# Kernel tuning notes

Hardware: AMD Instinct MI355X
Metric: run time of the kernel (lower is better)

The kernel has to match this reference:

```python
import jax, jax.numpy as jnp
import numpy as np

B, N, NC, T, C, H = 8, 16, 16, 64, 512, 8


def setup_inputs() -> dict:
    key = jax.random.key(0)
    ks = jax.random.split(key, 7)
    s = 1.0 / np.sqrt(C)  # ~kaiming-uniform scale for Linear weights
    x = jax.random.normal(ks[0], (B, N, T, C), dtype=jnp.float32)
    c = jax.random.normal(ks[1], (B, NC, T, C), dtype=jnp.float32)
    mask = jax.random.randint(ks[2], (B, N * T, (N + NC) * T), 0, 2).astype(bool)
    Wq = jax.random.normal(ks[3], (C, C), dtype=jnp.float32) * s  # [out, in], torch Linear layout
    Wk = jax.random.normal(ks[4], (C, C), dtype=jnp.float32) * s
    Wv = jax.random.normal(ks[5], (C, C), dtype=jnp.float32) * s
    Wp = jax.random.normal(ks[6], (C, C), dtype=jnp.float32) * s
    return {"x": x, "c": c, "mask": mask, "Wq": Wq, "Wk": Wk, "Wv": Wv, "Wp": Wp}


def reference(x, c, mask, Wq, Wk, Wv, Wp):
    Bx, Nx, Tx, Cx = x.shape
    Dh = Cx // H
    kv_in = jnp.concatenate([x, c], axis=1)           # hybrid: [B, N+NC, T, C]
    Nk = kv_in.shape[1]
    # torch Linear: y = x @ W.T  -> einsum '...c,dc->...d'
    q = jnp.einsum('bntc,dc->bntd', x, Wq).reshape(Bx, Nx * Tx, H, Dh).transpose(0, 2, 1, 3)
    k = jnp.einsum('bntc,dc->bntd', kv_in, Wk).reshape(Bx, Nk * Tx, H, Dh).transpose(0, 2, 1, 3)
    v = jnp.einsum('bntc,dc->bntd', kv_in, Wv).reshape(Bx, Nk * Tx, H, Dh).transpose(0, 2, 1, 3)
    att = jnp.einsum('bhqd,bhkd->bhqk', q, k) * (1.0 / np.sqrt(Dh))  # [B,H,NT,NkT]
    att = jnp.where(mask[:, None, :, :], -jnp.inf, att)
    att = jax.nn.softmax(att, axis=-1)
    y = jnp.einsum('bhqk,bhkd->bhqd', att, v)          # [B,H,NT,Dh]
    y = y.transpose(0, 2, 1, 3).reshape(Bx, Nx * Tx, Cx)
    y = jnp.einsum('btc,dc->btd', y, Wp)
    return y.reshape(Bx, Nx, Tx, Cx)
```

## Files before the change

### kernel.cpp

```cpp
#include <hip/hip_runtime.h>
#include <hip/hip_bf16.h>
#include <stdint.h>

typedef __bf16 v8bf __attribute__((ext_vector_type(8)));
typedef short v4s __attribute__((ext_vector_type(4)));
typedef float f32x4 __attribute__((ext_vector_type(4)));
typedef float f32x2 __attribute__((ext_vector_type(2)));

__device__ __forceinline__ void gload_lds16(const void* g, void* l) {
    __builtin_amdgcn_global_load_lds(
        (const __attribute__((address_space(1))) void*)g,
        (__attribute__((address_space(3))) void*)l, 16, 0, 0);
}

__device__ __forceinline__ unsigned short f2bf(float f) {
    __hip_bfloat16 h = __float2bfloat16(f);
    return __builtin_bit_cast(unsigned short, h);
}

__device__ __forceinline__ float andf(float e, int m) {
    return __builtin_bit_cast(float, __builtin_bit_cast(unsigned int, e) & (unsigned int)m);
}

__device__ __forceinline__ int sbit(unsigned int w, int off) {
    int m;
    asm("v_bfe_i32 %0, %1, %2, 1" : "=v"(m) : "v"(w), "v"(off));
    return m;
}

#define WAITV4_BAR() asm volatile("s_waitcnt vmcnt(4)\n\ts_barrier" ::: "memory")
#define WAITV0_BAR() asm volatile("s_waitcnt vmcnt(0)\n\ts_barrier" ::: "memory")
#define RAW_BAR() asm volatile("s_barrier" ::: "memory")

__device__ __forceinline__ f32x4 mfma16x16x16bf(v4s a, v4s b, f32x4 c) {
#if __has_builtin(__builtin_amdgcn_mfma_f32_16x16x16bf16_1k)
    return __builtin_amdgcn_mfma_f32_16x16x16bf16_1k(a, b, c, 0, 0, 0);
#elif __has_builtin(__builtin_amdgcn_mfma_f32_16x16x16_bf16)
    return __builtin_amdgcn_mfma_f32_16x16x16_bf16(a, b, c, 0, 0, 0);
#else
    asm("s_nop 1\n\t"
        "v_mfma_f32_16x16x16_bf16 %0, %1, %2, %0\n\t"
        "s_nop 7\n\ts_nop 3"
        : "+v"(c) : "v"(a), "v"(b));
    return c;
#endif
}

__global__ __launch_bounds__(256) void cvt_xcw(const float* __restrict__ x,
                                               const float* __restrict__ c,
                                               const float* __restrict__ wq,
                                               const float* __restrict__ wk,
                                               const float* __restrict__ wv,
                                               const float* __restrict__ wp,
                                               __hip_bfloat16* __restrict__ xc,
                                               __hip_bfloat16* __restrict__ wout) {
    int bid = blockIdx.x;
    if (bid < 8192) {
        int i = bid * 256 + threadIdx.x;
        long e = (long)i * 4;
        int b = (int)(e >> 20);
        int rem = (int)(e & ((1 << 20) - 1));
        int r = rem >> 9;
        int col = rem & 511;
        const float* src = (r < 1024) ? (x + ((long)b << 19) + (long)r * 512 + col)
                                      : (c + ((long)b << 19) + (long)(r - 1024) * 512 + col);
        float4 v = *(const float4*)src;
        ushort4 o;
        o.x = f2bf(v.x); o.y = f2bf(v.y); o.z = f2bf(v.z); o.w = f2bf(v.w);
        ((ushort4*)xc)[i] = o;
    } else {
        int i = (bid - 8192) * 256 + threadIdx.x;
        int e = i * 4;
        int w = e >> 18;
        int off = e & ((1 << 18) - 1);
        const float* src = (w == 0 ? wq : w == 1 ? wk : w == 2 ? wv : wp) + off;
        float4 val = *(const float4*)src;
        ushort4 o;
        o.x = f2bf(val.x); o.y = f2bf(val.y); o.z = f2bf(val.z); o.w = f2bf(val.w);
        ((ushort4*)wout)[i] = o;
    }
}

__global__ __launch_bounds__(256) void cvt_mask(const int* __restrict__ mask,
                                                unsigned long long* __restrict__ mbt) {
    int t = threadIdx.x;
    long base = (long)blockIdx.x * 1024;
#pragma unroll
    for (int j = 0; j < 4; j++) {
        long i = base + j * 256 + t;
        int v = mask[i] == 0;
        unsigned long long bits = __ballot(v);
        if ((t & 63) == 0) {
            int b = (int)(i >> 21);
            int q = (int)((i >> 11) & 1023);
            int word = (int)((i >> 6) & 31);
            mbt[((long)b * 32 + word) * 1024 + q] = bits;
        }
    }
}

__global__ __launch_bounds__(256) void gemm_qkv(const __hip_bfloat16* __restrict__ A,
                                                const __hip_bfloat16* __restrict__ Bw,
                                                __hip_bfloat16* __restrict__ Qw,
                                                __hip_bfloat16* __restrict__ Kw,
                                                __hip_bfloat16* __restrict__ Vtw) {
    __shared__ union {
        struct { __hip_bfloat16 As[2][128 * 32]; __hip_bfloat16 Bs[2][128 * 32]; } s;
        __hip_bfloat16 T[64 * 138];
    } u;
    const int tid = threadIdx.x;
    const int wave = tid >> 6, lane = tid & 63;
    const int m0 = blockIdx.x * 128, n0 = blockIdx.y * 128;

    const bool isQ = (blockIdx.y < 4);
    const int rr_base = m0 & 2047;
    if (isQ && rr_base >= 1024) return;

    const int la = lane >> 2;
    const int kc = (lane & 3) * 8;
    const long ga0 = (long)(m0 + wave * 16 + la) * 512 + kc;
    const long ga1 = (long)(m0 + (wave + 4) * 16 + la) * 512 + kc;
    const long gb0 = (long)(n0 + wave * 16 + la) * 512 + kc;
    const long gb1 = (long)(n0 + (wave + 4) * 16 + la) * 512 + kc;

    f32x4 acc[4][4] = {};
    const int mw = (wave & 1) * 64, nw = (wave >> 1) * 64;
    const int lrow = lane & 15, lk = (lane >> 4) * 8;

    gload_lds16(A + ga0, &u.s.As[0][wave * 512]);
    gload_lds16(A + ga1, &u.s.As[0][(wave + 4) * 512]);
    gload_lds16(Bw + gb0, &u.s.Bs[0][wave * 512]);
    gload_lds16(Bw + gb1, &u.s.Bs[0][(wave + 4) * 512]);

    for (int it = 0; it < 16; ++it) {
        const int cur = it & 1;
        if (it < 15) {
            const int k0 = (it + 1) * 32;
            gload_lds16(A + ga0 + k0, &u.s.As[cur ^ 1][wave * 512]);
            gload_lds16(A + ga1 + k0, &u.s.As[cur ^ 1][(wave + 4) * 512]);
            gload_lds16(Bw + gb0 + k0, &u.s.Bs[cur ^ 1][wave * 512]);
            gload_lds16(Bw + gb1 + k0, &u.s.Bs[cur ^ 1][(wave + 4) * 512]);
            WAITV4_BAR();
        } else {
            WAITV0_BAR();
        }
        v8bf a[4], b[4];
#pragma unroll
        for (int i = 0; i < 4; i++) {
            a[i] = *(const v8bf*)&u.s.As[cur][(mw + i * 16 + lrow) * 32 + lk];
            b[i] = *(const v8bf*)&u.s.Bs[cur][(nw + i * 16 + lrow) * 32 + lk];
        }
        __builtin_amdgcn_s_setprio(1);
#pragma unroll
        for (int mi = 0; mi < 4; mi++)
#pragma unroll
            for (int ni = 0; ni < 4; ni++)
                acc[mi][ni] = __builtin_amdgcn_mfma_f32_16x16x32_bf16(a[mi], b[ni], acc[mi][ni], 0, 0, 0);
        __builtin_amdgcn_s_setprio(0);
        RAW_BAR();
    }

    const int lq = lane >> 4;
    const int b_ = m0 >> 11;
    if (blockIdx.y < 8) {
        const float qs = isQ ? 0.1803368801f : 1.f;
#pragma unroll
        for (int pass = 0; pass < 2; ++pass) {
            if (pass) __syncthreads();
            if ((wave & 1) == pass) {
#pragma unroll
                for (int mi = 0; mi < 4; mi++)
#pragma unroll
                    for (int ni = 0; ni < 4; ni++) {
                        const int nl = nw + ni * 16 + lrow;
#pragma unroll
                        for (int r = 0; r < 4; r++)
                            u.T[(mi * 16 + lq * 4 + r) * 138 + nl] =
                                __float2bfloat16(acc[mi][ni][r] * qs);
                    }
            }
            __syncthreads();
#pragma unroll
            for (int i = 0; i < 4; i++) {
                int sI = tid + i * 256;
                int row = sI >> 4, ch = sI & 15;
                int grow = m0 + pass * 64 + row;
                int rr = grow & 2047;
                int gcol = n0 + ch * 8;
                int h = (gcol & 511) >> 6, dh = gcol & 63;
                uint4 v = *(const uint4*)&u.T[row * 138 + ch * 8];
                if (isQ)
                    *(uint4*)&Qw[((long)(b_ * 8 + h) * 1024 + rr) * 64 + dh] = v;
                else
                    *(uint4*)&Kw[((long)(b_ * 8 + h) * 2048 + rr) * 64 + dh] = v;
            }
        }
    } else {
        const int no = (blockIdx.y - 8) * 128;
        const int rrb = m0 & 2047;
#pragma unroll
        for (int pass = 0; pass < 2; ++pass) {
            __syncthreads();
            if ((wave >> 1) == pass) {
#pragma unroll
                for (int mi = 0; mi < 4; mi++)
#pragma unroll
                    for (int ni = 0; ni < 4; ni++) {
                        int n_l = ni * 16 + lrow;
                        int m_l = mw + mi * 16 + lq * 4;
                        ushort4 pk;
                        pk.x = f2bf(acc[mi][ni][0]); pk.y = f2bf(acc[mi][ni][1]);
                        pk.z = f2bf(acc[mi][ni][2]); pk.w = f2bf(acc[mi][ni][3]);
                        *(ushort4*)&u.T[n_l * 136 + m_l] = pk;
                    }
            }
            __syncthreads();
#pragma unroll
            for (int i = 0; i < 4; i++) {
                int sI = tid + i * 256;
                int n_l = sI >> 4, ch = sI & 15;
                int ng = no + pass * 64 + n_l;
                int h = ng >> 6, dh = ng & 63;
                uint4 v = *(const uint4*)&u.T[n_l * 136 + ch * 8];
                *(uint4*)&Vtw[((long)(b_ * 8 + h) * 64 + dh) * 2048 + rrb + ch * 8] = v;
            }
        }
    }
}

__global__ __launch_bounds__(256) void gemm_out(const __hip_bfloat16* __restrict__ A,
                                                const __hip_bfloat16* __restrict__ Bw,
                                                float* __restrict__ outp) {
    __shared__ __hip_bfloat16 As[2][128 * 32];
    __shared__ __hip_bfloat16 Bs[2][128 * 32];
    const int tid = threadIdx.x;
    const int wave = tid >> 6, lane = tid & 63;
    const int m0 = blockIdx.x * 128, n0 = blockIdx.y * 128;

    const int la = lane >> 2;
    const int kc = (lane & 3) * 8;
    const long ga0 = (long)(m0 + wave * 16 + la) * 512 + kc;
    const long ga1 = (long)(m0 + (wave + 4) * 16 + la) * 512 + kc;
    const long gb0 = (long)(n0 + wave * 16 + la) * 512 + kc;
    const long gb1 = (long)(n0 + (wave + 4) * 16 + la) * 512 + kc;

    f32x4 acc[4][4] = {};
    const int mw = (wave & 1) * 64, nw = (wave >> 1) * 64;
    const int lrow = lane & 15, lk = (lane >> 4) * 8;

    gload_lds16(A + ga0, &As[0][wave * 512]);
    gload_lds16(A + ga1, &As[0][(wave + 4) * 512]);
    gload_lds16(Bw + gb0, &Bs[0][wave * 512]);
    gload_lds16(Bw + gb1, &Bs[0][(wave + 4) * 512]);

    for (int it = 0; it < 16; ++it) {
        const int cur = it & 1;
        if (it < 15) {
            const int k0 = (it + 1) * 32;
            gload_lds16(A + ga0 + k0, &As[cur ^ 1][wave * 512]);
            gload_lds16(A + ga1 + k0, &As[cur ^ 1][(wave + 4) * 512]);
            gload_lds16(Bw + gb0 + k0, &Bs[cur ^ 1][wave * 512]);
            gload_lds16(Bw + gb1 + k0, &Bs[cur ^ 1][(wave + 4) * 512]);
            WAITV4_BAR();
        } else {
            WAITV0_BAR();
        }
        v8bf a[4], b[4];
#pragma unroll
        for (int i = 0; i < 4; i++) {
            a[i] = *(const v8bf*)&As[cur][(mw + i * 16 + lrow) * 32 + lk];
            b[i] = *(const v8bf*)&Bs[cur][(nw + i * 16 + lrow) * 32 + lk];
        }
        __builtin_amdgcn_s_setprio(1);
#pragma unroll
        for (int mi = 0; mi < 4; mi++)
#pragma unroll
            for (int ni = 0; ni < 4; ni++)
                acc[mi][ni] = __builtin_amdgcn_mfma_f32_16x16x32_bf16(a[mi], b[ni], acc[mi][ni], 0, 0, 0);
        __builtin_amdgcn_s_setprio(0);
        RAW_BAR();
    }

    const int lq = lane >> 4;
#pragma unroll
    for (int mi = 0; mi < 4; mi++)
#pragma unroll
        for (int ni = 0; ni < 4; ni++)
#pragma unroll
            for (int r = 0; r < 4; r++) {
                int grow = m0 + mw + mi * 16 + lq * 4 + r;
                int gcol = n0 + nw + ni * 16 + lrow;
                outp[(long)grow * 512 + gcol] = acc[mi][ni][r];
            }
}

__global__ __launch_bounds__(256) void flash(const __hip_bfloat16* __restrict__ Q,
                                             const __hip_bfloat16* __restrict__ K,
                                             const __hip_bfloat16* __restrict__ Vt,
                                             const unsigned long long* __restrict__ Mbt,
                                             __hip_bfloat16* __restrict__ Y) {
    constexpr int LDT = 72;
    __shared__ __hip_bfloat16 Ks[2][64 * LDT];
    __shared__ __hip_bfloat16 Vts[2][64 * LDT];

    const int L = blockIdx.x;
    const int b = L & 7, qt = (L >> 3) & 15, h = L >> 7;
    const int bh = b * 8 + h;
    const int tid = threadIdx.x, w = tid >> 6, lane = tid & 63;
    const int lcol = lane & 15, lq = lane >> 4;

    const __hip_bfloat16* Qp = Q + ((long)bh * 1024 + qt * 64 + w * 16 + lcol) * 64 + lq * 8;
    const __hip_bfloat16* Kg = K + (long)bh * 2048 * 64;
    const __hip_bfloat16* Vg = Vt + (long)bh * 64 * 2048;
    const unsigned long long* Mp = Mbt + (long)b * 32 * 1024 + qt * 64 + w * 16 + lcol;

    const int u0 = tid, u1 = tid + 256;
    const int r0 = u0 >> 3, p0 = u0 & 7;
    const int r1 = u1 >> 3, p1 = u1 & 7;

    int boff[8];
#pragma unroll
    for (int jj = 0; jj < 8; jj++)
        boff[jj] = (jj >> 2) * 16 + lq * 4 + (jj & 3);

    v8bf bq0 = *(const v8bf*)(Qp);
    v8bf bq1 = *(const v8bf*)(Qp + 32);

    f32x4 O[4] = {};
    f32x2 ls = {0.f, 0.f};

    unsigned long long mword = Mp[0];
    {
        const uint4* ksrc = (const uint4*)Kg;
        uint4 k0 = ksrc[u0], k1 = ksrc[u1];
        uint4 v0 = *(const uint4*)(Vg + (long)r0 * 2048 + p0 * 8);
        uint4 v1 = *(const uint4*)(Vg + (long)r1 * 2048 + p1 * 8);
        *(uint4*)&Ks[0][r0 * LDT + p0 * 8] = k0;
        *(uint4*)&Ks[0][r1 * LDT + p1 * 8] = k1;
        *(uint4*)&Vts[0][r0 * LDT + p0 * 8] = v0;
        *(uint4*)&Vts[0][r1 * LDT + p1 * 8] = v1;
    }
    __syncthreads();

    int cur = 0;
    for (int kt = 0; kt < 32; kt++) {
        const unsigned int kw_lo = (unsigned int)mword;
        const unsigned int kw_hi = (unsigned int)(mword >> 32);

        uint4 nk0, nk1, nv0, nv1;
        if (kt < 31) {
            const uint4* ksrc = (const uint4*)(Kg + ((kt + 1) << 12));
            nk0 = ksrc[u0];
            nk1 = ksrc[u1];
            nv0 = *(const uint4*)(Vg + (long)r0 * 2048 + (kt + 1) * 64 + p0 * 8);
            nv1 = *(const uint4*)(Vg + (long)r1 * 2048 + (kt + 1) * 64 + p1 * 8);
            mword = Mp[(long)(kt + 1) * 1024];
        }

        const __hip_bfloat16* Kb = Ks[cur];
        const __hip_bfloat16* Vb = Vts[cur];
#pragma unroll
        for (int nt = 0; nt < 4; nt++) {
            v8bf ak0 = *(const v8bf*)&Kb[(nt * 16 + lcol) * LDT + lq * 8];
            v8bf ak1 = *(const v8bf*)&Kb[(nt * 16 + lcol) * LDT + 32 + lq * 8];
            f32x4 st = {};
            __builtin_amdgcn_s_setprio(1);
            st = __builtin_amdgcn_mfma_f32_16x16x32_bf16(ak0, bq0, st, 0, 0, 0);
            st = __builtin_amdgcn_mfma_f32_16x16x32_bf16(ak1, bq1, st, 0, 0, 0);
            __builtin_amdgcn_s_setprio(0);
            const unsigned int kw = (nt < 2) ? kw_lo : kw_hi;
            const int base = (nt & 1) * 4;
            float e0 = andf(__builtin_amdgcn_exp2f(st[0]), sbit(kw, boff[base + 0]));
            float e1 = andf(__builtin_amdgcn_exp2f(st[1]), sbit(kw, boff[base + 1]));
            float e2 = andf(__builtin_amdgcn_exp2f(st[2]), sbit(kw, boff[base + 2]));
            float e3 = andf(__builtin_amdgcn_exp2f(st[3]), sbit(kw, boff[base + 3]));
            ls += (f32x2){e0, e1} + (f32x2){e2, e3};
            __hip_bfloat162 lo = __float22bfloat162_rn(make_float2(e0, e1));
            __hip_bfloat162 hi = __float22bfloat162_rn(make_float2(e2, e3));
            uint2 pku;
            __builtin_memcpy(&pku.x, &lo, 4);
            __builtin_memcpy(&pku.y, &hi, 4);
            v4s pa = __builtin_bit_cast(v4s, pku);
            __builtin_amdgcn_s_setprio(1);
#pragma unroll
            for (int nd = 0; nd < 4; nd++) {
                v4s bv = *(const v4s*)&Vb[(nd * 16 + lcol) * LDT + nt * 16 + lq * 4];
                O[nd] = mfma16x16x16bf(pa, bv, O[nd]);
            }
            __builtin_amdgcn_s_setprio(0);
        }

        if (kt < 31) {
            __hip_bfloat16* Kw_ = Ks[cur ^ 1];
            __hip_bfloat16* Vw_ = Vts[cur ^ 1];
            *(uint4*)&Kw_[r0 * LDT + p0 * 8] = nk0;
            *(uint4*)&Kw_[r1 * LDT + p1 * 8] = nk1;
            *(uint4*)&Vw_[r0 * LDT + p0 * 8] = nv0;
            *(uint4*)&Vw_[r1 * LDT + p1 * 8] = nv1;
        }
        __syncthreads();
        cur ^= 1;
    }

    float s = ls[0] + ls[1];
    s += __shfl_xor(s, 16);
    s += __shfl_xor(s, 32);
    float inv[4];
#pragma unroll
    for (int r = 0; r < 4; r++) inv[r] = 1.f / __shfl(s, lq * 4 + r);

    __hip_bfloat16* Yp = Y + ((long)b * 1024 + qt * 64 + w * 16) * 512 + h * 64 + lcol;
#pragma unroll
    for (int nd = 0; nd < 4; nd++)
#pragma unroll
        for (int r = 0; r < 4; r++)
            Yp[(long)(lq * 4 + r) * 512 + nd * 16] = __float2bfloat16(O[nd][r] * inv[r]);
}

extern "C" void kernel_launch(void* const* d_in, const int* in_sizes, int n_in,
                              void* d_out, int out_size, void* d_ws, size_t ws_size,
                              hipStream_t stream) {
    const float* x = (const float*)d_in[0];
    const float* c = (const float*)d_in[1];
    const int* mask = (const int*)d_in[2];
    const float* Wq = (const float*)d_in[3];
    const float* Wk = (const float*)d_in[4];
    const float* Wv = (const float*)d_in[5];
    const float* Wp = (const float*)d_in[6];

    char* ws = (char*)d_ws;
    __hip_bfloat16* xc  = (__hip_bfloat16*)(ws);
    __hip_bfloat16* Wbf = (__hip_bfloat16*)(ws + 16777216);
    __hip_bfloat16* Qw  = (__hip_bfloat16*)(ws + 18874368);
    __hip_bfloat16* Kw  = (__hip_bfloat16*)(ws + 27262976);
    __hip_bfloat16* Vtw = (__hip_bfloat16*)(ws + 44040192);
    __hip_bfloat16* Yb  = (__hip_bfloat16*)(ws + 60817408);
    unsigned long long* Mbp = (unsigned long long*)(ws);

    cvt_xcw<<<9216, 256, 0, stream>>>(x, c, Wq, Wk, Wv, Wp, xc, Wbf);
    gemm_qkv<<<dim3(128, 12), 256, 0, stream>>>(xc, Wbf, Qw, Kw, Vtw);
    cvt_mask<<<16384, 256, 0, stream>>>(mask, Mbp);
    flash<<<1024, 256, 0, stream>>>(Qw, Kw, Vtw, Mbp, Yb);
    gemm_out<<<dim3(64, 4), 256, 0, stream>>>(Yb, Wbf + 3 * 262144, (float*)d_out);
}
```

Before: 260.2 us.

## Double query rows per flash block to share K/V tiles across eight waves

The attention kernel now launches 512 blocks of 512 threads, each covering 128 query rows instead of 64, so each K/V tile staged in shared memory serves twice as many queries. Each thread now loads one 16-byte K and one V chunk per tile instead of two. This halves global K/V traffic for the flash stage and the per-thread staging work. In exchange, blocks are larger with more barrier participants, and there are fewer blocks to spread across compute units.

```diff
diff --git a/kernel.cpp b/kernel.cpp
--- a/kernel.cpp
+++ b/kernel.cpp
@@ -294,7 +294,7 @@
             }
 }
 
-__global__ __launch_bounds__(256) void flash(const __hip_bfloat16* __restrict__ Q,
+__global__ __launch_bounds__(512) void flash(const __hip_bfloat16* __restrict__ Q,
                                              const __hip_bfloat16* __restrict__ K,
                                              const __hip_bfloat16* __restrict__ Vt,
                                              const unsigned long long* __restrict__ Mbt,
@@ -304,19 +304,19 @@
     __shared__ __hip_bfloat16 Vts[2][64 * LDT];
 
     const int L = blockIdx.x;
-    const int b = L & 7, qt = (L >> 3) & 15, h = L >> 7;
+    const int b = L & 7, qt2 = (L >> 3) & 7, h = L >> 6;
     const int bh = b * 8 + h;
     const int tid = threadIdx.x, w = tid >> 6, lane = tid & 63;
     const int lcol = lane & 15, lq = lane >> 4;
-
-    const __hip_bfloat16* Qp = Q + ((long)bh * 1024 + qt * 64 + w * 16 + lcol) * 64 + lq * 8;
+    const int qrow = qt2 * 128 + w * 16;
+
+    const __hip_bfloat16* Qp = Q + ((long)bh * 1024 + qrow + lcol) * 64 + lq * 8;
     const __hip_bfloat16* Kg = K + (long)bh * 2048 * 64;
     const __hip_bfloat16* Vg = Vt + (long)bh * 64 * 2048;
-    const unsigned long long* Mp = Mbt + (long)b * 32 * 1024 + qt * 64 + w * 16 + lcol;
-
-    const int u0 = tid, u1 = tid + 256;
-    const int r0 = u0 >> 3, p0 = u0 & 7;
-    const int r1 = u1 >> 3, p1 = u1 & 7;
+    const unsigned long long* Mp = Mbt + (long)b * 32 * 1024 + qrow + lcol;
+
+    const int r0 = tid >> 3, p0 = tid & 7;
+    const __hip_bfloat16* Vp0 = Vg + (long)r0 * 2048 + p0 * 8;
 
     int boff[8];
 #pragma unroll
@@ -331,14 +331,10 @@
 
     unsigned long long mword = Mp[0];
     {
-        const uint4* ksrc = (const uint4*)Kg;
-        uint4 k0 = ksrc[u0], k1 = ksrc[u1];
-        uint4 v0 = *(const uint4*)(Vg + (long)r0 * 2048 + p0 * 8);
-        uint4 v1 = *(const uint4*)(Vg + (long)r1 * 2048 + p1 * 8);
+        uint4 k0 = ((const uint4*)Kg)[tid];
+        uint4 v0 = *(const uint4*)(Vp0);
         *(uint4*)&Ks[0][r0 * LDT + p0 * 8] = k0;
-        *(uint4*)&Ks[0][r1 * LDT + p1 * 8] = k1;
         *(uint4*)&Vts[0][r0 * LDT + p0 * 8] = v0;
-        *(uint4*)&Vts[0][r1 * LDT + p1 * 8] = v1;
     }
     __syncthreads();
 
@@ -347,13 +343,10 @@
         const unsigned int kw_lo = (unsigned int)mword;
         const unsigned int kw_hi = (unsigned int)(mword >> 32);
 
-        uint4 nk0, nk1, nv0, nv1;
+        uint4 nk0, nv0;
         if (kt < 31) {
-            const uint4* ksrc = (const uint4*)(Kg + ((kt + 1) << 12));
-            nk0 = ksrc[u0];
-            nk1 = ksrc[u1];
-            nv0 = *(const uint4*)(Vg + (long)r0 * 2048 + (kt + 1) * 64 + p0 * 8);
-            nv1 = *(const uint4*)(Vg + (long)r1 * 2048 + (kt + 1) * 64 + p1 * 8);
+            nk0 = ((const uint4*)(Kg + ((kt + 1) << 12)))[tid];
+            nv0 = *(const uint4*)(Vp0 + (kt + 1) * 64);
             mword = Mp[(long)(kt + 1) * 1024];
         }
 
@@ -391,12 +384,8 @@
         }
 
         if (kt < 31) {
-            __hip_bfloat16* Kw_ = Ks[cur ^ 1];
-            __hip_bfloat16* Vw_ = Vts[cur ^ 1];
-            *(uint4*)&Kw_[r0 * LDT + p0 * 8] = nk0;
-            *(uint4*)&Kw_[r1 * LDT + p1 * 8] = nk1;
-            *(uint4*)&Vw_[r0 * LDT + p0 * 8] = nv0;
-            *(uint4*)&Vw_[r1 * LDT + p1 * 8] = nv1;
+            *(uint4*)&Ks[cur ^ 1][r0 * LDT + p0 * 8] = nk0;
+            *(uint4*)&Vts[cur ^ 1][r0 * LDT + p0 * 8] = nv0;
         }
         __syncthreads();
         cur ^= 1;
@@ -409,7 +398,7 @@
 #pragma unroll
     for (int r = 0; r < 4; r++) inv[r] = 1.f / __shfl(s, lq * 4 + r);
 
-    __hip_bfloat16* Yp = Y + ((long)b * 1024 + qt * 64 + w * 16) * 512 + h * 64 + lcol;
+    __hip_bfloat16* Yp = Y + ((long)b * 1024 + qrow) * 512 + h * 64 + lcol;
 #pragma unroll
     for (int nd = 0; nd < 4; nd++)
 #pragma unroll
@@ -440,6 +429,6 @@
     cvt_xcw<<<9216, 256, 0, stream>>>(x, c, Wq, Wk, Wv, Wp, xc, Wbf);
     gemm_qkv<<<dim3(128, 12), 256, 0, stream>>>(xc, Wbf, Qw, Kw, Vtw);
     cvt_mask<<<16384, 256, 0, stream>>>(mask, Mbp);
-    flash<<<1024, 256, 0, stream>>>(Qw, Kw, Vtw, Mbp, Yb);
+    flash<<<512, 512, 0, stream>>>(Qw, Kw, Vtw, Mbp, Yb);
     gemm_out<<<dim3(64, 4), 256, 0, stream>>>(Yb, Wbf + 3 * 262144, (float*)d_out);
 }
```

Measured after the change: 251.9 us. 1.03x faster.
